# Kernel optimization log

Measured on AMD Instinct MI355X. Metric: run time of the kernel, lower is better.

## Reference

```python
import jax, jax.numpy as jnp
import numpy as np

B, C, H, W = 16, 256, 128, 128  # ration = 1 -> C' = C


def setup_inputs() -> dict:
    key = jax.random.key(0)
    ks = jax.random.split(key, 7)
    s = 1.0 / np.sqrt(C)
    return {
        "x": jax.random.normal(ks[0], (B, C, H, W), dtype=jnp.float32),
        "Wq": jax.random.normal(ks[1], (C, C), dtype=jnp.float32) * s,
        "Wk": jax.random.normal(ks[2], (C, C), dtype=jnp.float32) * s,
        "Wv": jax.random.normal(ks[3], (C, C), dtype=jnp.float32) * s,
        "gamma": jax.random.normal(ks[4], (1,), dtype=jnp.float32) * 0.1,
        "Wup": jax.random.normal(ks[5], (C, C), dtype=jnp.float32) * s,
        "b_up": jax.random.normal(ks[6], (C,), dtype=jnp.float32) * 0.01,
    }


def reference(x, Wq, Wk, Wv, gamma, Wup, b_up):
    b, c, h, w = x.shape
    # 1x1 conv (no bias) == channel-mixing einsum, followed by ReLU
    proj = lambda Wm: jax.nn.relu(jnp.einsum('oc,bchw->bohw', Wm, x))
    # torch .view(B, H, -1) is a raw row-major reinterpretation of [B,C,H,W]
    q = proj(Wq).reshape(b, h, -1)                      # [B, H, C*W]
    k = proj(Wk).reshape(b, h, -1).transpose(0, 2, 1)   # [B, C*W, H]
    v = proj(Wv).reshape(b, h, -1).transpose(0, 2, 1)   # [B, C*W, H]
    # non-standard softmax over dim=1 (rows of the HxH score matrix)
    attn = jax.nn.softmax(jnp.matmul(q, k), axis=1)     # [B, H, H]
    out1 = jnp.matmul(v, attn)                          # [B, C*W, H]
    out_h = out1.reshape(b, c, h, w) * gamma            # raw reshape, gamma scale
    # layer_up: 1x1 conv with bias
    out_h = jnp.einsum('oc,bchw->bohw', Wup, out_h) + b_up[None, :, None, None]
    return (out_h, q, k, v, gamma, attn)
```

## Files before the change

### kernel.cpp

```cpp
#include <hip/hip_runtime.h>
#include <stdint.h>


typedef _Float16 f16;
typedef __attribute__((ext_vector_type(8))) _Float16 f16x8;
typedef __attribute__((ext_vector_type(4))) float f32x4;

#define DEV static __device__ __forceinline__

constexpr int  HW   = 16384;
constexpr long PB   = 4194304;
constexpr long HALF = 2097152;

constexpr long WH_OFF  = 0;
constexpr long WL_OFF  = 393216;
constexpr long WU_OFF  = 786432;
constexpr long WS_NEED = 1048576;

DEV unsigned pk2(float a, float b) {
  auto h = __builtin_amdgcn_cvt_pkrtz(a, b);
  return __builtin_bit_cast(unsigned, h);
}
DEV void split_pk2(float a, float b, unsigned& hu, unsigned& lu) {
  auto h = __builtin_amdgcn_cvt_pkrtz(a, b);
  auto l = __builtin_amdgcn_cvt_pkrtz(a - (float)h[0], b - (float)h[1]);
  hu = __builtin_bit_cast(unsigned, h);
  lu = __builtin_bit_cast(unsigned, l);
}
DEV f32x4 mfma16(f16x8 a, f16x8 b, f32x4 c) {
  return __builtin_amdgcn_mfma_f32_16x16x32_f16(a, b, c, 0, 0, 0);
}
DEV f16x8 ld64(const char* base, int row, int g) {
  return *(const f16x8*)(base + row * 64 + 16 * (g ^ ((row >> 1) & 3)));
}

DEV void gload16(const void* g, void* l) {
  __builtin_amdgcn_global_load_lds(
      (const __attribute__((address_space(1))) uint32_t*)(g),
      (__attribute__((address_space(3))) uint32_t*)(l), 16, 0, 0);
}

DEV int swz(int row, int kbyte) {
  return (kbyte & ~63) | ((kbyte & 63) ^ (((row >> 3) & 3) << 4));
}
DEV f16x8 ldfrag(const f16* arr, int strideB, int row, int kbyte) {
  return *(const f16x8*)((const char*)arr + row * strideB + swz(row, kbyte));
}

__global__ __launch_bounds__(256) void prep_w(
    const float* __restrict__ Wq, const float* __restrict__ Wk,
    const float* __restrict__ Wv, const float* __restrict__ Wu,
    const float* __restrict__ gin, char* __restrict__ ws) {
  const int kc = blockIdx.x, m = blockIdx.y, o = threadIdx.x;
  const float* src = (m == 0) ? Wq : (m == 1) ? Wk : (m == 2) ? Wv : Wu;
  const float sc = (m == 3) ? gin[0] : 1.0f;
  float v[32];
#pragma unroll
  for (int j = 0; j < 32; ++j) v[j] = src[o * 256 + kc * 32 + j] * sc;
  char* dh = (m < 3) ? (ws + WH_OFF + ((long)(m * 8 + kc) * 256 + o) * 64)
                     : (ws + WU_OFF + ((long)kc * 256 + o) * 64);
  char* dl = ws + WL_OFF + ((long)(m * 8 + kc) * 256 + o) * 64;
  const int sw = (o >> 1) & 3;
#pragma unroll
  for (int gq = 0; gq < 4; ++gq) {
    unsigned h[4], l[4];
#pragma unroll
    for (int p = 0; p < 4; ++p)
      split_pk2(v[8 * gq + 2 * p], v[8 * gq + 2 * p + 1], h[p], l[p]);
    const int off = 16 * (gq ^ sw);
    *(uint4*)(dh + off) = make_uint4(h[0], h[1], h[2], h[3]);
    if (m < 3) *(uint4*)(dl + off) = make_uint4(l[0], l[1], l[2], l[3]);
  }
}

__global__ __launch_bounds__(512, 4) void qkv_fused4(
    const float* __restrict__ x,
    const char* __restrict__ wqh, const char* __restrict__ wql,
    const char* __restrict__ wkh, const char* __restrict__ wkl,
    const char* __restrict__ wvh,
    float* __restrict__ qseg, float* __restrict__ kseg,
    float* __restrict__ vseg) {
  __shared__ char lds[65536];
  char* Xh = lds;
  char* Xl = lds + 32768;
  float* R = (float*)(lds + 32768);
  const int t = threadIdx.x, lane = t & 63, w = t >> 6;
  const int l15 = lane & 15, g = lane >> 4;
  const int b = blockIdx.y, hw0 = blockIdx.x * 64;
  const float* xb = x + (long)b * PB + hw0;

  {
    const int hw = t & 63, cq = t >> 6;
    const int sw = (hw >> 1) & 3;
#pragma unroll
    for (int j8 = 0; j8 < 4; ++j8) {
      const int c0 = cq * 32 + j8 * 8;
      float v[8];
#pragma unroll
      for (int i = 0; i < 8; ++i) v[i] = xb[(long)(c0 + i) * HW + hw];
      unsigned h[4], l[4];
#pragma unroll
      for (int p = 0; p < 4; ++p)
        split_pk2(v[2 * p], v[2 * p + 1], h[p], l[p]);
      const int kc = cq, gi = j8;
      const int off = kc * 4096 + hw * 64 + 16 * (gi ^ sw);
      *(uint4*)(Xh + off) = make_uint4(h[0], h[1], h[2], h[3]);
      *(uint4*)(Xl + off) = make_uint4(l[0], l[1], l[2], l[3]);
    }
  }
  __syncthreads();

  auto repack_store = [&](f32x4 (&ac)[4][2], float* ob) {
#pragma unroll
    for (int half = 0; half < 2; ++half) {
#pragma unroll
      for (int mf2 = 0; mf2 < 2; ++mf2) {
        const int mf = 2 * half + mf2;
#pragma unroll
        for (int nf = 0; nf < 2; ++nf)
#pragma unroll
          for (int r = 0; r < 4; ++r) {
            const int hwloc = 16 * mf2 + 4 * g + r;
            const int o = w * 32 + 16 * nf + l15;
            const int col = (o >> 1) ^ (((hwloc >> 2) & 3) << 3);
            float v = ac[mf][nf][r];
            R[(o & 1) * 4096 + hwloc * 128 + col] = v > 0.f ? v : 0.f;
          }
      }
      __syncthreads();
#pragma unroll
      for (int it = 0; it < 4; ++it) {
        const int f = t + 512 * it;
        const int parity = f >> 10, hwloc = (f >> 5) & 31, q4 = f & 31;
        const int col = (4 * q4) ^ (((hwloc >> 2) & 3) << 3);
        const float4 v4 = *(const float4*)(R + parity * 4096 + hwloc * 128 + col);
        *(float4*)(ob + (long)parity * HALF +
                   (long)(hw0 + 32 * half + hwloc) * 128 + 4 * q4) = v4;
      }
      __syncthreads();
    }
  };

  {
    f32x4 acc[2][4] = {};
    for (int kc = 0; kc < 8; ++kc) {
      const char* XH = Xh + kc * 4096;
      const char* XL = Xl + kc * 4096;
      const char* WH = wqh + (long)kc * 16384;
      const char* WL = wql + (long)kc * 16384;
      f16x8 bh[4], bl[4];
#pragma unroll
      for (int nf = 0; nf < 4; ++nf) {
        bh[nf] = ld64(XH, 16 * nf + l15, g);
        bl[nf] = ld64(XL, 16 * nf + l15, g);
      }
#pragma unroll
      for (int mf = 0; mf < 2; ++mf) {
        const int orow = w * 32 + 16 * mf + l15;
        f16x8 ah = ld64(WH, orow, g);
        f16x8 al = ld64(WL, orow, g);
#pragma unroll
        for (int nf = 0; nf < 4; ++nf) {
          acc[mf][nf] = mfma16(ah, bh[nf], acc[mf][nf]);
          acc[mf][nf] = mfma16(ah, bl[nf], acc[mf][nf]);
          acc[mf][nf] = mfma16(al, bh[nf], acc[mf][nf]);
        }
      }
    }
    float* ob = qseg + (long)b * PB;
#pragma unroll
    for (int mf = 0; mf < 2; ++mf)
#pragma unroll
      for (int nf = 0; nf < 4; ++nf)
#pragma unroll
        for (int r = 0; r < 4; ++r) {
          float v = acc[mf][nf][r];
          v = v > 0.f ? v : 0.f;
          const int o = w * 32 + 16 * mf + 4 * g + r;
          const int hw = hw0 + 16 * nf + l15;
          ob[(long)o * HW + hw] = v;
        }
  }

  {
    f32x4 acc[4][2] = {};
    for (int kc = 0; kc < 8; ++kc) {
      const char* XH = Xh + kc * 4096;
      const char* XL = Xl + kc * 4096;
      const char* WH = wkh + (long)kc * 16384;
      const char* WL = wkl + (long)kc * 16384;
      f16x8 bh[2], bl[2];
#pragma unroll
      for (int nf = 0; nf < 2; ++nf) {
        const int orow = w * 32 + 16 * nf + l15;
        bh[nf] = ld64(WH, orow, g);
        bl[nf] = ld64(WL, orow, g);
      }
#pragma unroll
      for (int mf = 0; mf < 4; ++mf) {
        f16x8 ah = ld64(XH, 16 * mf + l15, g);
        f16x8 al = ld64(XL, 16 * mf + l15, g);
#pragma unroll
        for (int nf = 0; nf < 2; ++nf) {
          acc[mf][nf] = mfma16(ah, bh[nf], acc[mf][nf]);
          acc[mf][nf] = mfma16(ah, bl[nf], acc[mf][nf]);
          acc[mf][nf] = mfma16(al, bh[nf], acc[mf][nf]);
        }
      }
    }
    __syncthreads();
    repack_store(acc, kseg + (long)b * PB);
  }

  {
    f32x4 acc[4][2] = {};
    for (int kc = 0; kc < 8; ++kc) {
      const char* XH = Xh + kc * 4096;
      const char* WH = wvh + (long)kc * 16384;
      f16x8 bh[2];
#pragma unroll
      for (int nf = 0; nf < 2; ++nf)
        bh[nf] = ld64(WH, w * 32 + 16 * nf + l15, g);
#pragma unroll
      for (int mf = 0; mf < 4; ++mf) {
        f16x8 ah = ld64(XH, 16 * mf + l15, g);
#pragma unroll
        for (int nf = 0; nf < 2; ++nf)
          acc[mf][nf] = mfma16(ah, bh[nf], acc[mf][nf]);
      }
    }
    repack_store(acc, vseg + (long)b * PB);
  }
}

__global__ __launch_bounds__(256) void spart_kernel(
    const float* __restrict__ qseg, const float* __restrict__ kseg,
    float* __restrict__ part) {
  constexpr int SB = 80;
  __shared__ f16 Ah[128 * 40], Al[128 * 40], Bh[128 * 40], Bl[128 * 40];
  const int t = threadIdx.x, lane = t & 63, w = t >> 6;
  const int l15 = lane & 15, g = lane >> 4;
  const int ch = blockIdx.x, b = blockIdx.y;
  const float* qb = qseg + (long)b * PB + ch * 1024;
  const float* kb = kseg + (long)b * PB + (long)ch * 1024 * 128;

  f32x4 acc[4][4] = {};

  for (int kc = 0; kc < 1024; kc += 32) {
#pragma unroll
    for (int it = 0; it < 4; ++it) {
      int f4 = t + 256 * it;
      int i = f4 >> 3, c4 = f4 & 7;
      float4 v = *(const float4*)(qb + (long)i * 32768 + kc + 4 * c4);
      unsigned h01, l01, h23, l23;
      split_pk2(v.x, v.y, h01, l01);
      split_pk2(v.z, v.w, h23, l23);
      int kbo = swz(i, 8 * c4);
      *(uint2*)((char*)Ah + i * SB + kbo) = make_uint2(h01, h23);
      *(uint2*)((char*)Al + i * SB + kbo) = make_uint2(l01, l23);
    }
    {
      int c = t & 127, rh = t >> 7;
      float vs[16];
#pragma unroll
      for (int r = 0; r < 16; ++r)
        vs[r] = kb[(long)(kc + 16 * rh + r) * 128 + c];
#pragma unroll
      for (int u = 0; u < 4; ++u) {
        unsigned h0, l0, h1, l1;
        split_pk2(vs[4 * u], vs[4 * u + 1], h0, l0);
        split_pk2(vs[4 * u + 2], vs[4 * u + 3], h1, l1);
        int kbo = swz(c, 32 * rh + 8 * u);
        *(uint2*)((char*)Bh + c * SB + kbo) = make_uint2(h0, h1);
        *(uint2*)((char*)Bl + c * SB + kbo) = make_uint2(l0, l1);
      }
    }
    __syncthreads();

    f16x8 afh[4], afl[4], bfh[4], bfl[4];
#pragma unroll
    for (int f = 0; f < 4; ++f) {
      int ar = (w & 1) * 64 + 16 * f + l15;
      int br = (w >> 1) * 64 + 16 * f + l15;
      afh[f] = ldfrag(Ah, SB, ar, 16 * g);
      afl[f] = ldfrag(Al, SB, ar, 16 * g);
      bfh[f] = ldfrag(Bh, SB, br, 16 * g);
      bfl[f] = ldfrag(Bl, SB, br, 16 * g);
    }
#pragma unroll
    for (int mf = 0; mf < 4; ++mf)
#pragma unroll
      for (int nf = 0; nf < 4; ++nf) {
        acc[mf][nf] = mfma16(afh[mf], bfh[nf], acc[mf][nf]);
        acc[mf][nf] = mfma16(afh[mf], bfl[nf], acc[mf][nf]);
        acc[mf][nf] = mfma16(afl[mf], bfh[nf], acc[mf][nf]);
      }
    __syncthreads();
  }

  float* pp = part + (long)(b * 32 + ch) * 16384;
#pragma unroll
  for (int mf = 0; mf < 4; ++mf)
#pragma unroll
    for (int nf = 0; nf < 4; ++nf)
#pragma unroll
      for (int r = 0; r < 4; ++r) {
        int i = (w & 1) * 64 + 16 * mf + 4 * g + r;
        int i2 = (w >> 1) * 64 + 16 * nf + l15;
        pp[i * 128 + i2] = acc[mf][nf][r];
      }
}

__global__ __launch_bounds__(128) void reduce_s(
    const float* __restrict__ part, float* __restrict__ att,
    float* __restrict__ gout, const float* __restrict__ gin) {
  const int i = blockIdx.x, b = blockIdx.y, t = threadIdx.x;
  if (b == 0 && i == 0 && t == 0) gout[0] = gin[0];
  const float* pp = part + (long)b * 524288 + i * 128 + t;
  float s = 0.f;
#pragma unroll
  for (int c = 0; c < 32; ++c) s += pp[(long)c * 16384];
  att[((long)b * 128 + i) * 128 + t] = s;
}

__global__ __launch_bounds__(256) void softmax2(float* __restrict__ att) {
  __shared__ float red[16][17];
  const int b = blockIdx.y, c0 = blockIdx.x * 16;
  const int t = threadIdx.x, col = t & 15, ig = t >> 4;
  float* ab = att + (long)b * 16384 + c0 + col;
  float s[8];
  float m = -3.0e38f;
#pragma unroll
  for (int j = 0; j < 8; ++j) {
    s[j] = ab[(ig * 8 + j) * 128];
    m = fmaxf(m, s[j]);
  }
  red[ig][col] = m;
  __syncthreads();
  float mx = red[0][col];
#pragma unroll
  for (int k = 1; k < 16; ++k) mx = fmaxf(mx, red[k][col]);
  float sum = 0.f;
#pragma unroll
  for (int j = 0; j < 8; ++j) {
    s[j] = expf(s[j] - mx);
    sum += s[j];
  }
  __syncthreads();
  red[ig][col] = sum;
  __syncthreads();
  float tot = 0.f;
#pragma unroll
  for (int k = 0; k < 16; ++k) tot += red[k][col];
  float inv = 1.f / tot;
#pragma unroll
  for (int j = 0; j < 8; ++j) ab[(ig * 8 + j) * 128] = s[j] * inv;
}

__global__ __launch_bounds__(256, 2) void pvf_fused(
    const float* __restrict__ vseg, const float* __restrict__ att,
    const char* __restrict__ wu, const float* __restrict__ bup,
    float* __restrict__ oseg) {
  __shared__ char attnT[128 * 272];
  __shared__ char vA[64 * 272];
  __shared__ char HT[128 * 144];
  const int t = threadIdx.x, lane = t & 63, w = t >> 6;
  const int l15 = lane & 15, g = lane >> 4;
  const int b = blockIdx.y, h = blockIdx.x;
  const float* ab = att + (long)b * 16384;
  const float* vb = vseg + (long)b * PB;
  float* Ob = oseg + (long)b * PB;

#pragma unroll
  for (int it = 0; it < 4; ++it) {
    const int f = t + 256 * it;
    const int i4 = f >> 5, w4 = f & 31;
    const float4 r0 = *(const float4*)(ab + (4 * i4 + 0) * 128 + 4 * w4);
    const float4 r1 = *(const float4*)(ab + (4 * i4 + 1) * 128 + 4 * w4);
    const float4 r2 = *(const float4*)(ab + (4 * i4 + 2) * 128 + 4 * w4);
    const float4 r3 = *(const float4*)(ab + (4 * i4 + 3) * 128 + 4 * w4);
    *(uint2*)(attnT + (4 * w4 + 0) * 272 + swz(4 * w4 + 0, 8 * i4)) =
        make_uint2(pk2(r0.x, r1.x), pk2(r2.x, r3.x));
    *(uint2*)(attnT + (4 * w4 + 1) * 272 + swz(4 * w4 + 1, 8 * i4)) =
        make_uint2(pk2(r0.y, r1.y), pk2(r2.y, r3.y));
    *(uint2*)(attnT + (4 * w4 + 2) * 272 + swz(4 * w4 + 2, 8 * i4)) =
        make_uint2(pk2(r0.z, r1.z), pk2(r2.z, r3.z));
    *(uint2*)(attnT + (4 * w4 + 3) * 272 + swz(4 * w4 + 3, 8 * i4)) =
        make_uint2(pk2(r0.w, r1.w), pk2(r2.w, r3.w));
  }

  f32x4 acc2[4][8] = {};

  for (int cc = 0; cc < 4; ++cc) {
#pragma unroll
    for (int it = 0; it < 8; ++it) {
      const int f = t + 256 * it;
      const int cp = f >> 5, q4 = f & 31;
      const float4 v4 =
          *(const float4*)(vb + ((long)(cc * 64 + cp) * 128 + h) * 128 + 4 * q4);
      *(uint2*)(vA + cp * 272 + swz(cp, 8 * q4)) =
          make_uint2(pk2(v4.x, v4.y), pk2(v4.z, v4.w));
    }
    __syncthreads();

    f32x4 acc1[8] = {};
#pragma unroll
    for (int kf = 0; kf < 4; ++kf) {
      const f16x8 a = ldfrag((const f16*)vA, 272, w * 16 + l15, 64 * kf + 16 * g);
#pragma unroll
      for (int nf = 0; nf < 8; ++nf) {
        const f16x8 bf = ldfrag((const f16*)attnT, 272, 16 * nf + l15, 64 * kf + 16 * g);
        acc1[nf] = mfma16(a, bf, acc1[nf]);
      }
    }
#pragma unroll
    for (int nf = 0; nf < 8; ++nf)
#pragma unroll
      for (int r = 0; r < 4; ++r) {
        const int wp = 16 * nf + l15;
        const int cp = w * 16 + 4 * g + r;
        *(f16*)(HT + wp * 144 + swz(wp, 2 * cp)) = (f16)acc1[nf][r];
      }
    __syncthreads();

#pragma unroll
    for (int kf2 = 0; kf2 < 2; ++kf2) {
      const char* WU = wu + (long)(cc * 2 + kf2) * 16384;
      f16x8 af[4];
#pragma unroll
      for (int mf = 0; mf < 4; ++mf)
        af[mf] = ld64(WU, w * 64 + 16 * mf + l15, g);
#pragma unroll
      for (int nf = 0; nf < 8; ++nf) {
        const f16x8 bf = ldfrag((const f16*)HT, 144, 16 * nf + l15, 64 * kf2 + 16 * g);
#pragma unroll
        for (int mf = 0; mf < 4; ++mf)
          acc2[mf][nf] = mfma16(af[mf], bf, acc2[mf][nf]);
      }
    }
  }

#pragma unroll
  for (int mf = 0; mf < 4; ++mf)
#pragma unroll
    for (int nf = 0; nf < 8; ++nf)
#pragma unroll
      for (int r = 0; r < 4; ++r) {
        const int o = w * 64 + 16 * mf + 4 * g + r;
        const int wp = 16 * nf + l15;
        Ob[(long)o * HW + h * 128 + wp] = acc2[mf][nf][r] + bup[o];
      }
}

__global__ __launch_bounds__(128) void softmax_kernel(
    const float* __restrict__ part, float* __restrict__ att,
    float* __restrict__ gout, const float* __restrict__ gin) {
  const int b = blockIdx.x, t = threadIdx.x;
  if (b == 0 && t == 0) gout[0] = gin[0];
  const float* pp = part + (long)b * 32 * 16384;
  float* ab = att + (long)b * 16384;
  float mx = -3.0e38f;
  for (int i = 0; i < 128; ++i) {
    float s = 0.f;
#pragma unroll
    for (int c = 0; c < 32; ++c) s += pp[(long)c * 16384 + i * 128 + t];
    ab[i * 128 + t] = s;
    mx = fmaxf(mx, s);
  }
  float sum = 0.f;
  for (int i = 0; i < 128; ++i) {
    float e = expf(ab[i * 128 + t] - mx);
    sum += e;
    ab[i * 128 + t] = e;
  }
  float inv = 1.f / sum;
  for (int i = 0; i < 128; ++i) ab[i * 128 + t] *= inv;
}

template <int MODE>
__global__ __launch_bounds__(256) void proj_kernel(
    const float* __restrict__ x, const float* __restrict__ Wm,
    float* __restrict__ out) {
  constexpr int SB = 80;
  __shared__ f16 Wh[256 * 40];
  __shared__ f16 Wl[256 * 40];
  __shared__ f16 Xh[64 * 40];
  __shared__ f16 Xl[64 * 40];

  const int t = threadIdx.x;
  const int lane = t & 63;
  const int w = t >> 6;
  const int l15 = lane & 15;
  const int g = lane >> 4;
  const int b = blockIdx.y;
  const int hw0 = blockIdx.x * 64;
  const float* xb = x + (long)b * PB;

  f32x4 acc[4][4] = {};

  for (int kc = 0; kc < 256; kc += 32) {
#pragma unroll
    for (int it = 0; it < 8; ++it) {
      int f4 = t + 256 * it;
      int o = f4 >> 3, c4 = f4 & 7;
      float4 v = *(const float4*)(Wm + o * 256 + kc + 4 * c4);
      unsigned h01, l01, h23, l23;
      split_pk2(v.x, v.y, h01, l01);
      split_pk2(v.z, v.w, h23, l23);
      int kb = swz(o, 8 * c4);
      *(uint2*)((char*)Wh + o * SB + kb) = make_uint2(h01, h23);
      *(uint2*)((char*)Wl + o * SB + kb) = make_uint2(l01, l23);
    }
    {
      int c = t & 63, rq = t >> 6;
      float vs[8];
#pragma unroll
      for (int r = 0; r < 8; ++r)
        vs[r] = xb[(long)(kc + 8 * rq + r) * HW + hw0 + c];
#pragma unroll
      for (int u = 0; u < 2; ++u) {
        unsigned h0, l0, h1, l1;
        split_pk2(vs[4 * u], vs[4 * u + 1], h0, l0);
        split_pk2(vs[4 * u + 2], vs[4 * u + 3], h1, l1);
        int kb = swz(c, 16 * rq + 8 * u);
        *(uint2*)((char*)Xh + c * SB + kb) = make_uint2(h0, h1);
        *(uint2*)((char*)Xl + c * SB + kb) = make_uint2(l0, l1);
      }
    }
    __syncthreads();

    f16x8 wfh[4], wfl[4], xfh[4], xfl[4];
#pragma unroll
    for (int f = 0; f < 4; ++f) {
      int wr = 64 * w + 16 * f + l15;
      int xr = 16 * f + l15;
      wfh[f] = ldfrag(Wh, SB, wr, 16 * g);
      wfl[f] = ldfrag(Wl, SB, wr, 16 * g);
      xfh[f] = ldfrag(Xh, SB, xr, 16 * g);
      xfl[f] = ldfrag(Xl, SB, xr, 16 * g);
    }
#pragma unroll
    for (int mf = 0; mf < 4; ++mf)
#pragma unroll
      for (int nf = 0; nf < 4; ++nf) {
        if constexpr (MODE == 0) {
          acc[mf][nf] = mfma16(wfh[mf], xfh[nf], acc[mf][nf]);
          acc[mf][nf] = mfma16(wfh[mf], xfl[nf], acc[mf][nf]);
          acc[mf][nf] = mfma16(wfl[mf], xfh[nf], acc[mf][nf]);
        } else {
          acc[mf][nf] = mfma16(xfh[mf], wfh[nf], acc[mf][nf]);
          acc[mf][nf] = mfma16(xfh[mf], wfl[nf], acc[mf][nf]);
          acc[mf][nf] = mfma16(xfl[mf], wfh[nf], acc[mf][nf]);
        }
      }
    __syncthreads();
  }

  float* ob = out + (long)b * PB;
#pragma unroll
  for (int mf = 0; mf < 4; ++mf)
#pragma unroll
    for (int nf = 0; nf < 4; ++nf)
#pragma unroll
      for (int r = 0; r < 4; ++r) {
        float v = acc[mf][nf][r];
        v = v > 0.f ? v : 0.f;
        if constexpr (MODE == 0) {
          int o = 64 * w + 16 * mf + 4 * g + r;
          int hw = hw0 + 16 * nf + l15;
          ob[(long)o * HW + hw] = v;
        } else {
          int hw = hw0 + 16 * mf + 4 * g + r;
          int o = 64 * w + 16 * nf + l15;
          ob[((o & 1) ? HALF : 0) + (long)hw * 128 + (o >> 1)] = v;
        }
      }
}

__global__ __launch_bounds__(256) void out1_fb(
    const float* __restrict__ vseg, const float* __restrict__ att,
    float* __restrict__ outseg) {
  constexpr int SB = 272;
  __shared__ f16 Va[64 * 136], Ba[128 * 136];
  const int t = threadIdx.x, lane = t & 63, w = t >> 6;
  const int l15 = lane & 15, g = lane >> 4;
  const int b = blockIdx.y;
  const long j0 = (long)blockIdx.x * 64;
  const float* vb = vseg + (long)b * PB + j0 * 128;
  const float* ab = att + (long)b * 16384;

#pragma unroll
  for (int it = 0; it < 8; ++it) {
    int f4 = t + 256 * it;
    int j = f4 >> 5, c4 = f4 & 31;
    float4 v = *(const float4*)(vb + (long)j * 128 + 4 * c4);
    int kb = swz(j, 8 * c4);
    *(uint2*)((char*)Va + j * SB + kb) = make_uint2(pk2(v.x, v.y), pk2(v.z, v.w));
  }
  {
    int c = t & 127, rh = t >> 7;
#pragma unroll
    for (int uu = 0; uu < 16; ++uu) {
      int i0 = 64 * rh + 4 * uu;
      float v0 = ab[(i0 + 0) * 128 + c];
      float v1 = ab[(i0 + 1) * 128 + c];
      float v2 = ab[(i0 + 2) * 128 + c];
      float v3 = ab[(i0 + 3) * 128 + c];
      int kb = swz(c, 2 * i0);
      *(uint2*)((char*)Ba + c * SB + kb) = make_uint2(pk2(v0, v1), pk2(v2, v3));
    }
  }
  __syncthreads();

  f32x4 acc[2][4] = {};
#pragma unroll
  for (int kf = 0; kf < 4; ++kf) {
    f16x8 af[2], bf[4];
#pragma unroll
    for (int mf = 0; mf < 2; ++mf)
      af[mf] = ldfrag(Va, SB, (w & 1) * 32 + 16 * mf + l15, 64 * kf + 16 * g);
#pragma unroll
    for (int nf = 0; nf < 4; ++nf)
      bf[nf] = ldfrag(Ba, SB, (w >> 1) * 64 + 16 * nf + l15, 64 * kf + 16 * g);
#pragma unroll
    for (int mf = 0; mf < 2; ++mf)
#pragma unroll
      for (int nf = 0; nf < 4; ++nf)
        acc[mf][nf] = mfma16(af[mf], bf[nf], acc[mf][nf]);
  }

  float* ob = outseg + (long)b * PB;
#pragma unroll
  for (int mf = 0; mf < 2; ++mf)
#pragma unroll
    for (int nf = 0; nf < 4; ++nf)
#pragma unroll
      for (int r = 0; r < 4; ++r) {
        long j = j0 + (w & 1) * 32 + 16 * mf + 4 * g + r;
        int i2 = (w >> 1) * 64 + 16 * nf + l15;
        ob[j * 128 + i2] = acc[mf][nf][r];
      }
}

__global__ __launch_bounds__(256) void final_kernel(
    float* __restrict__ outseg, const float* __restrict__ Wup,
    const float* __restrict__ bup, const float* __restrict__ gin) {
  constexpr int SB = 144;
  __shared__ f16 Ah[256 * 72], Bh[64 * 72];
  const int t = threadIdx.x, lane = t & 63, w = t >> 6;
  const int l15 = lane & 15, g = lane >> 4;
  const int b = blockIdx.y;
  const int hw0 = blockIdx.x * 64;
  const float gamma = gin[0];
  float* Hb = outseg + (long)b * PB;

  f32x4 acc[4][4] = {};

  for (int kc = 0; kc < 256; kc += 64) {
#pragma unroll
    for (int it = 0; it < 16; ++it) {
      int f4 = t + 256 * it;
      int o = f4 >> 4, c4 = f4 & 15;
      float4 v = *(const float4*)(Wup + o * 256 + kc + 4 * c4);
      int kb = swz(o, 8 * c4);
      *(uint2*)((char*)Ah + o * SB + kb) =
          make_uint2(pk2(v.x * gamma, v.y * gamma), pk2(v.z * gamma, v.w * gamma));
    }
    {
      int n = t & 63, rq = t >> 6;
#pragma unroll
      for (int uu = 0; uu < 4; ++uu) {
        int r0 = 16 * rq + 4 * uu;
        float v0 = Hb[(long)(kc + r0 + 0) * HW + hw0 + n];
        float v1 = Hb[(long)(kc + r0 + 1) * HW + hw0 + n];
        float v2 = Hb[(long)(kc + r0 + 2) * HW + hw0 + n];
        float v3 = Hb[(long)(kc + r0 + 3) * HW + hw0 + n];
        int kb = swz(n, 2 * r0);
        *(uint2*)((char*)Bh + n * SB + kb) = make_uint2(pk2(v0, v1), pk2(v2, v3));
      }
    }
    __syncthreads();

    f16x8 af[4][2], bf[4][2];
#pragma unroll
    for (int f = 0; f < 4; ++f)
#pragma unroll
      for (int kf = 0; kf < 2; ++kf) {
        af[f][kf] = ldfrag(Ah, SB, 64 * w + 16 * f + l15, 64 * kf + 16 * g);
        bf[f][kf] = ldfrag(Bh, SB, 16 * f + l15, 64 * kf + 16 * g);
      }
#pragma unroll
    for (int mf = 0; mf < 4; ++mf)
#pragma unroll
      for (int nf = 0; nf < 4; ++nf) {
        acc[mf][nf] = mfma16(af[mf][0], bf[nf][0], acc[mf][nf]);
        acc[mf][nf] = mfma16(af[mf][1], bf[nf][1], acc[mf][nf]);
      }
    __syncthreads();
  }

#pragma unroll
  for (int mf = 0; mf < 4; ++mf)
#pragma unroll
    for (int nf = 0; nf < 4; ++nf)
#pragma unroll
      for (int r = 0; r < 4; ++r) {
        int o = 64 * w + 16 * mf + 4 * g + r;
        int hw = hw0 + 16 * nf + l15;
        Hb[(long)o * HW + hw] = acc[mf][nf][r] + bup[o];
      }
}

extern "C" void kernel_launch(void* const* d_in, const int* in_sizes, int n_in,
                              void* d_out, int out_size, void* d_ws, size_t ws_size,
                              hipStream_t stream) {
  (void)in_sizes; (void)n_in; (void)out_size;

  const float* x  = (const float*)d_in[0];
  const float* Wq = (const float*)d_in[1];
  const float* Wk = (const float*)d_in[2];
  const float* Wv = (const float*)d_in[3];
  const float* gm = (const float*)d_in[4];
  const float* Wu = (const float*)d_in[5];
  const float* bu = (const float*)d_in[6];

  float* out  = (float*)d_out;
  float* oseg = out;
  float* qseg = out + 67108864L;
  float* kseg = out + 134217728L;
  float* vseg = out + 201326592L;
  float* gseg = out + 268435456L;
  float* aseg = out + 268435457L;

  dim3 blk(256);
  if (ws_size >= (size_t)WS_NEED && d_ws != nullptr) {
    char* ws = (char*)d_ws;
    prep_w<<<dim3(8, 4), blk, 0, stream>>>(Wq, Wk, Wv, Wu, gm, ws);
    qkv_fused4<<<dim3(256, 16), dim3(512), 0, stream>>>(
        x, ws + WH_OFF, ws + WL_OFF, ws + WH_OFF + 131072, ws + WL_OFF + 131072,
        ws + WH_OFF + 262144, qseg, kseg, vseg);
    spart_kernel<<<dim3(32, 16), blk, 0, stream>>>(qseg, kseg, oseg);
    reduce_s<<<dim3(128, 16), dim3(128), 0, stream>>>(oseg, aseg, gseg, gm);
    softmax2<<<dim3(8, 16), blk, 0, stream>>>(aseg);
    pvf_fused<<<dim3(128, 16), blk, 0, stream>>>(vseg, aseg, ws + WU_OFF, bu, oseg);
  } else {
    proj_kernel<0><<<dim3(256, 16), blk, 0, stream>>>(x, Wq, qseg);
    proj_kernel<1><<<dim3(256, 16), blk, 0, stream>>>(x, Wk, kseg);
    proj_kernel<1><<<dim3(256, 16), blk, 0, stream>>>(x, Wv, vseg);
    spart_kernel<<<dim3(32, 16), blk, 0, stream>>>(qseg, kseg, oseg);
    softmax_kernel<<<dim3(16), dim3(128), 0, stream>>>(oseg, aseg, gseg, gm);
    out1_fb<<<dim3(512, 16), blk, 0, stream>>>(vseg, aseg, oseg);
    final_kernel<<<dim3(256, 16), blk, 0, stream>>>(oseg, Wu, bu, gm);
  }
}
```

Before: 633.5 us.

## Use 512-thread blocks in fused PV+up-proj kernel and prefetch next V chunk

The fused attention-apply and up-projection kernel now runs with 8 waves per block, splitting the 128 output columns between two wave halves so each wave holds half the accumulators. The V tile for the next channel chunk is loaded into registers while the current chunk's MFMAs run, hiding global load latency behind compute. The intent is more latency hiding and occupancy. In exchange each block issues more Wu fragment loads, and launch bounds of 4 blocks per CU may force register pressure or spills.

```diff
diff --git a/kernel.cpp b/kernel.cpp
--- a/kernel.cpp
+++ b/kernel.cpp
@@ -357,7 +357,7 @@
   for (int j = 0; j < 8; ++j) ab[(ig * 8 + j) * 128] = s[j] * inv;
 }
 
-__global__ __launch_bounds__(256, 2) void pvf_fused(
+__global__ __launch_bounds__(512, 4) void pvf2(
     const float* __restrict__ vseg, const float* __restrict__ att,
     const char* __restrict__ wu, const float* __restrict__ bup,
     float* __restrict__ oseg) {
@@ -366,14 +366,22 @@
   __shared__ char HT[128 * 144];
   const int t = threadIdx.x, lane = t & 63, w = t >> 6;
   const int l15 = lane & 15, g = lane >> 4;
+  const int wq = w & 3, wh = w >> 2;
   const int b = blockIdx.y, h = blockIdx.x;
   const float* ab = att + (long)b * 16384;
   const float* vb = vseg + (long)b * PB;
   float* Ob = oseg + (long)b * PB;
 
-#pragma unroll
-  for (int it = 0; it < 4; ++it) {
-    const int f = t + 256 * it;
+  const int s_cp = t >> 3;
+  const int s_q0 = (t & 7) * 4;
+  float4 vr[4];
+#pragma unroll
+  for (int it = 0; it < 4; ++it)
+    vr[it] = *(const float4*)(vb + ((long)(s_cp)*128 + h) * 128 + 4 * (s_q0 + it));
+
+#pragma unroll
+  for (int it = 0; it < 2; ++it) {
+    const int f = t + 512 * it;
     const int i4 = f >> 5, w4 = f & 31;
     const float4 r0 = *(const float4*)(ab + (4 * i4 + 0) * 128 + 4 * w4);
     const float4 r1 = *(const float4*)(ab + (4 * i4 + 1) * 128 + 4 * w4);
@@ -389,36 +397,44 @@
         make_uint2(pk2(r0.w, r1.w), pk2(r2.w, r3.w));
   }
 
-  f32x4 acc2[4][8] = {};
+  f32x4 acc2[4][4] = {};
 
   for (int cc = 0; cc < 4; ++cc) {
 #pragma unroll
-    for (int it = 0; it < 8; ++it) {
-      const int f = t + 256 * it;
-      const int cp = f >> 5, q4 = f & 31;
-      const float4 v4 =
-          *(const float4*)(vb + ((long)(cc * 64 + cp) * 128 + h) * 128 + 4 * q4);
-      *(uint2*)(vA + cp * 272 + swz(cp, 8 * q4)) =
-          make_uint2(pk2(v4.x, v4.y), pk2(v4.z, v4.w));
-    }
-    __syncthreads();
-
-    f32x4 acc1[8] = {};
+    for (int it = 0; it < 2; ++it) {
+      const int q4 = s_q0 + 2 * it;
+      *(uint4*)(vA + s_cp * 272 + swz(s_cp, 8 * q4)) = make_uint4(
+          pk2(vr[2 * it].x, vr[2 * it].y), pk2(vr[2 * it].z, vr[2 * it].w),
+          pk2(vr[2 * it + 1].x, vr[2 * it + 1].y),
+          pk2(vr[2 * it + 1].z, vr[2 * it + 1].w));
+    }
+    __syncthreads();
+
+    float4 vn[4];
+    if (cc < 3) {
+#pragma unroll
+      for (int it = 0; it < 4; ++it)
+        vn[it] = *(const float4*)(
+            vb + ((long)((cc + 1) * 64 + s_cp) * 128 + h) * 128 + 4 * (s_q0 + it));
+    }
+
+    f32x4 acc1[4] = {};
 #pragma unroll
     for (int kf = 0; kf < 4; ++kf) {
-      const f16x8 a = ldfrag((const f16*)vA, 272, w * 16 + l15, 64 * kf + 16 * g);
-#pragma unroll
-      for (int nf = 0; nf < 8; ++nf) {
-        const f16x8 bf = ldfrag((const f16*)attnT, 272, 16 * nf + l15, 64 * kf + 16 * g);
+      const f16x8 a = ldfrag((const f16*)vA, 272, wq * 16 + l15, 64 * kf + 16 * g);
+#pragma unroll
+      for (int nf = 0; nf < 4; ++nf) {
+        const f16x8 bf = ldfrag((const f16*)attnT, 272, wh * 64 + 16 * nf + l15,
+                                64 * kf + 16 * g);
         acc1[nf] = mfma16(a, bf, acc1[nf]);
       }
     }
 #pragma unroll
-    for (int nf = 0; nf < 8; ++nf)
+    for (int nf = 0; nf < 4; ++nf)
 #pragma unroll
       for (int r = 0; r < 4; ++r) {
-        const int wp = 16 * nf + l15;
-        const int cp = w * 16 + 4 * g + r;
+        const int wp = wh * 64 + 16 * nf + l15;
+        const int cp = wq * 16 + 4 * g + r;
         *(f16*)(HT + wp * 144 + swz(wp, 2 * cp)) = (f16)acc1[nf][r];
       }
     __syncthreads();
@@ -429,25 +445,30 @@
       f16x8 af[4];
 #pragma unroll
       for (int mf = 0; mf < 4; ++mf)
-        af[mf] = ld64(WU, w * 64 + 16 * mf + l15, g);
-#pragma unroll
-      for (int nf = 0; nf < 8; ++nf) {
-        const f16x8 bf = ldfrag((const f16*)HT, 144, 16 * nf + l15, 64 * kf2 + 16 * g);
+        af[mf] = ld64(WU, wq * 64 + 16 * mf + l15, g);
+#pragma unroll
+      for (int nf = 0; nf < 4; ++nf) {
+        const f16x8 bf = ldfrag((const f16*)HT, 144, wh * 64 + 16 * nf + l15,
+                                64 * kf2 + 16 * g);
 #pragma unroll
         for (int mf = 0; mf < 4; ++mf)
           acc2[mf][nf] = mfma16(af[mf], bf, acc2[mf][nf]);
       }
     }
+    if (cc < 3) {
+#pragma unroll
+      for (int it = 0; it < 4; ++it) vr[it] = vn[it];
+    }
   }
 
 #pragma unroll
   for (int mf = 0; mf < 4; ++mf)
 #pragma unroll
-    for (int nf = 0; nf < 8; ++nf)
+    for (int nf = 0; nf < 4; ++nf)
 #pragma unroll
       for (int r = 0; r < 4; ++r) {
-        const int o = w * 64 + 16 * mf + 4 * g + r;
-        const int wp = 16 * nf + l15;
+        const int o = wq * 64 + 16 * mf + 4 * g + r;
+        const int wp = wh * 64 + 16 * nf + l15;
         Ob[(long)o * HW + h * 128 + wp] = acc2[mf][nf][r] + bup[o];
       }
 }
@@ -742,7 +763,7 @@
     spart_kernel<<<dim3(32, 16), blk, 0, stream>>>(qseg, kseg, oseg);
     reduce_s<<<dim3(128, 16), dim3(128), 0, stream>>>(oseg, aseg, gseg, gm);
     softmax2<<<dim3(8, 16), blk, 0, stream>>>(aseg);
-    pvf_fused<<<dim3(128, 16), blk, 0, stream>>>(vseg, aseg, ws + WU_OFF, bu, oseg);
+    pvf2<<<dim3(128, 16), dim3(512), 0, stream>>>(vseg, aseg, ws + WU_OFF, bu, oseg);
   } else {
     proj_kernel<0><<<dim3(256, 16), blk, 0, stream>>>(x, Wq, qseg);
     proj_kernel<1><<<dim3(256, 16), blk, 0, stream>>>(x, Wk, kseg);
```

Result: slower. 691.0 us (+9.1%).
